# Performance work log

Hardware: AMD Instinct MI355X
Metric: run time of the kernel (lower is better)

## Reference

```python
import jax, jax.numpy as jnp
import numpy as np

B, S = 2, 2048
DIM_IN, DIM_OUT, NUM_HEADS, DIM_QK = 1024, 128, 16, 128


def setup_inputs() -> dict:
    key = jax.random.key(0)
    k0, k1, k2, k3 = jax.random.split(key, 4)
    x = jax.random.normal(k0, (B, S, DIM_IN), jnp.float32)
    mask = jax.random.bernoulli(k1, 0.1, (B, S))  # True = masked-out token
    # xavier-normal-ish scales (exact init values are irrelevant for correctness)
    std_in = float(np.sqrt(2.0 / (NUM_HEADS * DIM_QK + DIM_IN * DIM_QK)))
    proj_in = jax.random.normal(k2, (DIM_IN, NUM_HEADS, 2 * DIM_QK + DIM_OUT), jnp.float32) * std_in
    v_bias = jnp.zeros((NUM_HEADS, DIM_OUT), jnp.float32)
    std_out = float(np.sqrt(2.0 / (DIM_OUT * DIM_OUT + NUM_HEADS * DIM_OUT)))
    proj_out = jax.random.normal(k3, (NUM_HEADS, DIM_OUT, DIM_OUT), jnp.float32) * std_out
    proj_out_bias = jnp.zeros((DIM_OUT,), jnp.float32)
    return {"x": x, "mask": mask, "proj_in": proj_in, "v_bias": v_bias,
            "proj_out": proj_out, "proj_out_bias": proj_out_bias}


def _rotary(t):
    # t: [z, s, h, d]; GPT-NeoX style rotary as in the torch Rotary module
    d = t.shape[-1]
    half = -(-d // 2)  # ceil(d/2), matches torch.arange(0,-1,-2/d)
    freq_half = 10000.0 ** (jnp.arange(half, dtype=jnp.float32) * (-2.0 / d))
    freq = jnp.concatenate([freq_half, freq_half[: half - d % 2]])  # length d
    pos = jnp.arange(t.shape[1], dtype=jnp.float32)
    ang = pos[:, None] * freq[None, :]             # [s, d]
    cos = jnp.cos(ang)[None, :, None, :]
    sin = jnp.sin(ang)[None, :, None, :]
    x1, x2 = jnp.split(t, 2, axis=-1)
    rot = jnp.concatenate([-x2, x1], axis=-1)
    return t * cos + rot * sin


def _inf_cube(t):
    return t ** 3


def reference(x, mask, proj_in, v_bias, proj_out, proj_out_bias):
    qkv = jnp.einsum('zki,iho->zkho', x, proj_in)
    q, k, v = jnp.split(qkv, [DIM_QK, 2 * DIM_QK], axis=-1)
    q = _rotary(q)
    k = _rotary(k)
    scores = jnp.einsum('zqha,zkha->zqkh', q, k) / jnp.sqrt(jnp.float32(DIM_QK))
    # dual mask: row (query) OR column (key) masked -> -inf
    m = jnp.logical_or(mask[:, :, None, None], mask[:, None, :, None])  # [z,q,k,1]
    scores = jnp.where(m, -jnp.inf, scores)
    attn = jnp.nan_to_num(jax.nn.softmax(scores, axis=2))  # softmax over k; nan rows -> 0
    o = jnp.einsum('zqkh,zkhx->zqhx', attn, v + v_bias[None, None])
    out = jnp.einsum('zqhx,hxy->zqy', _inf_cube(o), proj_out) + proj_out_bias[None, None]
    return _inf_cube(out)
```

## Files before the change

kernel.cpp:

```cpp
#include <hip/hip_runtime.h>
#include <math.h>

#define BZ 2
#define SQ 2048
#define DIN 1024
#define HH 16
#define NT 6144
#define MROWS 4096
#define KOUT 2048
#define KSPLIT 8

typedef unsigned short u16t;
typedef unsigned int u32t;
typedef __attribute__((ext_vector_type(8))) short bf16x8;
typedef __attribute__((ext_vector_type(4))) float f32x4;

__device__ __forceinline__ float cubef(float x) { return x * x * x; }

__device__ __forceinline__ u16t f2bf(float f) {
    u32t b = __float_as_uint(f);
    b += 0x7FFFu + ((b >> 16) & 1u);
    return (u16t)(b >> 16);
}
__device__ __forceinline__ float bf2f(u16t u) { return __uint_as_float(((u32t)u) << 16); }
__device__ __forceinline__ u32t pk2(float a, float b) {
    return (u32t)f2bf(a) | ((u32t)f2bf(b) << 16);
}

__global__ __launch_bounds__(256) void bf16_x(const float* __restrict__ x,
                                              u16t* __restrict__ xb) {
    const size_t idx = ((size_t)blockIdx.x * 256 + threadIdx.x) * 8;
    float4 f0 = *(const float4*)&x[idx];
    float4 f1 = *(const float4*)&x[idx + 4];
    u32t h[4];
    h[0] = pk2(f0.x, f0.y); h[1] = pk2(f0.z, f0.w);
    h[2] = pk2(f1.x, f1.y); h[3] = pk2(f1.z, f1.w);
    *(uint4*)&xb[idx] = *(uint4*)&h[0];
}

__global__ __launch_bounds__(256) void transpose_w(const float* __restrict__ W,
                                                   u16t* __restrict__ Th) {
    __shared__ float tile[64][68];
    const int n0 = blockIdx.x * 64;
    const int k0 = blockIdx.y * 64;
    const int t = threadIdx.x;
    {
        const int r = t >> 4, c = (t & 15) * 4;
        #pragma unroll
        for (int p = 0; p < 4; p++) {
            float4 v = *(const float4*)&W[(size_t)(k0 + r + p * 16) * NT + n0 + c];
            *(float4*)&tile[r + p * 16][c] = v;
        }
    }
    __syncthreads();
    const int nr = t >> 2;
    const int kc = (t & 3) * 16;
    u32t hi[8];
    #pragma unroll
    for (int j = 0; j < 8; j++)
        hi[j] = pk2(tile[kc + 2 * j][nr], tile[kc + 2 * j + 1][nr]);
    size_t ob = (size_t)(n0 + nr) * DIN + k0 + kc;
    *(uint4*)&Th[ob]     = *(uint4*)&hi[0];
    *(uint4*)&Th[ob + 8] = *(uint4*)&hi[4];
}

__global__ __launch_bounds__(256) void transpose_w2(const float* __restrict__ W,
                                                    u16t* __restrict__ Th) {
    __shared__ float tile[64][68];
    const int n0 = blockIdx.x * 64;
    const int k0 = blockIdx.y * 64;
    const int t = threadIdx.x;
    {
        const int r = t >> 4, c = (t & 15) * 4;
        #pragma unroll
        for (int p = 0; p < 4; p++) {
            float4 v = *(const float4*)&W[(size_t)(k0 + r + p * 16) * 128 + n0 + c];
            *(float4*)&tile[r + p * 16][c] = v;
        }
    }
    __syncthreads();
    const int nr = t >> 2;
    const int kc = (t & 3) * 16;
    u32t hi[8];
    #pragma unroll
    for (int j = 0; j < 8; j++)
        hi[j] = pk2(tile[kc + 2 * j][nr], tile[kc + 2 * j + 1][nr]);
    size_t ob = (size_t)(n0 + nr) * KOUT + k0 + kc;
    *(uint4*)&Th[ob]     = *(uint4*)&hi[0];
    *(uint4*)&Th[ob + 8] = *(uint4*)&hi[4];
}

__global__ __launch_bounds__(256) void gemm_qkv3(const u16t* __restrict__ Ah,
                                                 const u16t* __restrict__ Bh,
                                                 const float* __restrict__ vb,
                                                 u16t* __restrict__ QB,
                                                 u16t* __restrict__ KB,
                                                 u16t* __restrict__ VF) {
    __shared__ __align__(16) u16t as_h[4 * 128 * 8];
    __shared__ __align__(16) u16t bs_h[4 * 128 * 8];

    const int t = threadIdx.x;
    const int lane = t & 63, wid = t >> 6;
    const int quad = lane >> 4, l15 = lane & 15;
    const int wm = (wid & 1) * 64;
    const int wn = (wid >> 1) * 64;
    const int tile = blockIdx.x;
    const int h = tile / 3, t3 = tile - h * 3;
    const int colBase = tile * 128;
    const int rowBase = blockIdx.y * 128;
    const int sm = t & 127;
    const int skh = t >> 7;

    f32x4 acc[4][4];
    #pragma unroll
    for (int i = 0; i < 4; i++)
        #pragma unroll
        for (int j = 0; j < 4; j++) acc[i][j] = (f32x4){0.f, 0.f, 0.f, 0.f};

    const u16t* aPtr = Ah + (size_t)(rowBase + sm) * DIN + skh * 16;
    const u16t* bPtr = Bh + (size_t)(colBase + sm) * DIN + skh * 16;
    u16t* aw = &as_h[(skh * 2) * 1024 + sm * 8];
    u16t* bw = &bs_h[(skh * 2) * 1024 + sm * 8];

    for (int k0 = 0; k0 < DIN; k0 += 32) {
        uint4 a0 = *(const uint4*)(aPtr + k0);
        uint4 a1 = *(const uint4*)(aPtr + k0 + 8);
        uint4 b0 = *(const uint4*)(bPtr + k0);
        uint4 b1 = *(const uint4*)(bPtr + k0 + 8);
        __syncthreads();
        *(uint4*)(aw)        = a0;
        *(uint4*)(aw + 1024) = a1;
        *(uint4*)(bw)        = b0;
        *(uint4*)(bw + 1024) = b1;
        __syncthreads();

        bf16x8 ah[4], bh[4];
        #pragma unroll
        for (int mt = 0; mt < 4; mt++)
            ah[mt] = *(const bf16x8*)&as_h[quad * 1024 + (wm + mt * 16 + l15) * 8];
        #pragma unroll
        for (int nt = 0; nt < 4; nt++)
            bh[nt] = *(const bf16x8*)&bs_h[quad * 1024 + (wn + nt * 16 + l15) * 8];
        #pragma unroll
        for (int mt = 0; mt < 4; mt++)
            #pragma unroll
            for (int nt = 0; nt < 4; nt++)
                acc[mt][nt] = __builtin_amdgcn_mfma_f32_16x16x32_bf16(ah[mt], bh[nt], acc[mt][nt], 0, 0, 0);
    }

    const int z = rowBase >> 11;
    const int s0 = (rowBase & 2047) + wm + quad * 4;
    const size_t obase = (size_t)(z * 16 + h) * 2048;
    if (t3 == 2) {
        #pragma unroll
        for (int nt = 0; nt < 4; nt++) {
            int c = wn + nt * 16 + l15;
            float bb = vb[h * 128 + c];
            #pragma unroll
            for (int mt = 0; mt < 4; mt++)
                #pragma unroll
                for (int r = 0; r < 4; r++)
                    VF[(obase + s0 + mt * 16 + r) * 128 + c] = f2bf(acc[mt][nt][r] + bb);
        }
    } else {
        u16t* dst = t3 ? KB : QB;
        #pragma unroll
        for (int nt = 0; nt < 4; nt++) {
            int c = wn + nt * 16 + l15;
            #pragma unroll
            for (int mt = 0; mt < 4; mt++)
                #pragma unroll
                for (int r = 0; r < 4; r++)
                    dst[(obase + s0 + mt * 16 + r) * 128 + c] = f2bf(acc[mt][nt][r]);
        }
    }
}

__global__ __launch_bounds__(256) void prep_rot_trans(u16t* __restrict__ QB,
                                                      u16t* __restrict__ KB,
                                                      u16t* __restrict__ VTh) {
    const int bx = blockIdx.x;
    const int st = bx & 63, h = (bx >> 6) & 15, z = bx >> 10;
    const int t = threadIdx.x;
    const size_t base = ((size_t)(z * 16 + h) * 2048 + st * 32) * 128;

    {
        const int r = t >> 3, w = t & 7;
        const int c = w & 3;
        const int s = st * 32 + r;
        u16t* buf = (w < 4) ? QB : KB;
        u16t* p1 = buf + base + (size_t)r * 128 + c * 16;
        u16t* p2 = p1 + 64;
        uint4 a0 = *(uint4*)p1, a1 = *(uint4*)(p1 + 8);
        uint4 b0 = *(uint4*)p2, b1 = *(uint4*)(p2 + 8);
        u32t A[8] = {a0.x, a0.y, a0.z, a0.w, a1.x, a1.y, a1.z, a1.w};
        u32t B[8] = {b0.x, b0.y, b0.z, b0.w, b1.x, b1.y, b1.z, b1.w};
        u32t OA[8], OB[8];
        #pragma unroll
        for (int p = 0; p < 8; p++) {
            float x1a = bf2f((u16t)(A[p] & 0xFFFFu)), x1b = bf2f((u16t)(A[p] >> 16));
            float x2a = bf2f((u16t)(B[p] & 0xFFFFu)), x2b = bf2f((u16t)(B[p] >> 16));
            int j0 = c * 16 + 2 * p;
            float f0 = expf(-0.14391156831212788f * (float)j0);
            float f1 = expf(-0.14391156831212788f * (float)(j0 + 1));
            float sn0, cs0, sn1, cs1;
            sincosf((float)s * f0, &sn0, &cs0);
            sincosf((float)s * f1, &sn1, &cs1);
            OA[p] = pk2(x1a * cs0 - x2a * sn0, x1b * cs1 - x2b * sn1);
            OB[p] = pk2(x2a * cs0 + x1a * sn0, x2b * cs1 + x1b * sn1);
        }
        *(uint4*)p1       = make_uint4(OA[0], OA[1], OA[2], OA[3]);
        *(uint4*)(p1 + 8) = make_uint4(OA[4], OA[5], OA[6], OA[7]);
        *(uint4*)p2       = make_uint4(OB[0], OB[1], OB[2], OB[3]);
        *(uint4*)(p2 + 8) = make_uint4(OB[4], OB[5], OB[6], OB[7]);
    }

    __shared__ u16t vt[128 * 40];
    {
        uint4 a = *(uint4*)(VTh + base + t * 16);
        uint4 b = *(uint4*)(VTh + base + t * 16 + 8);
        int row = t >> 3, d0 = (t & 7) * 16;
        u32t W[8] = {a.x, a.y, a.z, a.w, b.x, b.y, b.z, b.w};
        #pragma unroll
        for (int p = 0; p < 8; p++) {
            vt[(d0 + 2 * p) * 40 + row]     = (u16t)(W[p] & 0xFFFFu);
            vt[(d0 + 2 * p + 1) * 40 + row] = (u16t)(W[p] >> 16);
        }
    }
    __syncthreads();
    {
        int d = t >> 1, k0 = (t & 1) * 16;
        uint4 a = *(uint4*)&vt[d * 40 + k0];
        uint4 b = *(uint4*)&vt[d * 40 + k0 + 8];
        *(uint4*)(VTh + base + t * 16)     = a;
        *(uint4*)(VTh + base + t * 16 + 8) = b;
    }
}

#define ATTSCALE 0.08838834764831845f

__global__ __launch_bounds__(256, 4) void attn_kernel3(const u16t* __restrict__ QB,
                                                       const u16t* __restrict__ KB,
                                                       const u16t* __restrict__ VTh,
                                                       const int* __restrict__ mask,
                                                       u16t* __restrict__ O3b) {
    const int blk = blockIdx.x;
    const int qt = blk & 31;
    const int h  = (blk >> 5) & 15;
    const int z  = blk >> 9;
    const int t  = threadIdx.x;
    const int lane = t & 63, wid = t >> 6;
    const int quad = lane >> 4, l15 = lane & 15;
    const int w1 = wid & 1;
    const int kh = wid >> 1;

    __shared__ __align__(16) u16t ks[32 * 136];
    __shared__ __align__(16) u16t vth[128 * 40];
    __shared__ __align__(16) u16t wlb[64 * 40];
    __shared__ float dpart[2][64];
    __shared__ int qm[64], km[32];

    const int q0 = qt * 64;
    const size_t zh = (size_t)(z * 16 + h);
    const u16t* qb  = QB  + zh * 262144;
    const u16t* kb  = KB  + zh * 262144;
    const u16t* vhg = VTh + zh * 262144;

    bf16x8 qf[2][4];
    #pragma unroll
    for (int i = 0; i < 2; i++)
        #pragma unroll
        for (int kk = 0; kk < 4; kk++)
            qf[i][kk] = *(const bf16x8*)(qb + (size_t)(q0 + 16 * (w1 + 2 * i) + l15) * 128 + kk * 32 + quad * 8);
    if (t < 64) qm[t] = mask[z * SQ + q0 + t];

    f32x4 acc[2][4];
    #pragma unroll
    for (int i = 0; i < 2; i++)
        #pragma unroll
        for (int d = 0; d < 4; d++) acc[i][d] = (f32x4){0.f, 0.f, 0.f, 0.f};
    float dsum[2][4] = {{0.f, 0.f, 0.f, 0.f}, {0.f, 0.f, 0.f, 0.f}};

    for (int kt = 0; kt < SQ; kt += 32) {
        __syncthreads();
        {
            const u16t* src = kb + (size_t)kt * 128 + t * 16;
            uint4 a = *(const uint4*)(src);
            uint4 b = *(const uint4*)(src + 8);
            int row = t >> 3, co = (t & 7) * 16;
            *(uint4*)&ks[row * 136 + co]     = a;
            *(uint4*)&ks[row * 136 + co + 8] = b;
        }
        {
            const u16t* srch = vhg + (size_t)(kt >> 5) * 4096 + t * 16;
            uint4 a = *(const uint4*)(srch);
            uint4 b = *(const uint4*)(srch + 8);
            int dd = t >> 1, k0 = (t & 1) * 16;
            *(uint4*)&vth[dd * 40 + k0]     = a;
            *(uint4*)&vth[dd * 40 + k0 + 8] = b;
        }
        if (t < 32) km[t] = mask[z * SQ + kt + t];
        __syncthreads();

        f32x4 s4[2] = {(f32x4){0.f, 0.f, 0.f, 0.f}, (f32x4){0.f, 0.f, 0.f, 0.f}};
        #pragma unroll
        for (int kk = 0; kk < 4; kk++) {
            bf16x8 kf = *(const bf16x8*)&ks[(16 * kh + l15) * 136 + kk * 32 + quad * 8];
            s4[0] = __builtin_amdgcn_mfma_f32_16x16x32_bf16(qf[0][kk], kf, s4[0], 0, 0, 0);
            s4[1] = __builtin_amdgcn_mfma_f32_16x16x32_bf16(qf[1][kk], kf, s4[1], 0, 0, 0);
        }
        {
            int colm = km[16 * kh + l15];
            #pragma unroll
            for (int i = 0; i < 2; i++)
                #pragma unroll
                for (int r = 0; r < 4; r++) {
                    int row = 16 * (w1 + 2 * i) + 4 * quad + r;
                    float wv = (qm[row] | colm) ? 0.f : __expf(s4[i][r] * ATTSCALE);
                    dsum[i][r] += wv;
                    wlb[row * 40 + 16 * kh + l15] = f2bf(wv);
                }
        }
        __syncthreads();

        bf16x8 pa[2];
        #pragma unroll
        for (int i = 0; i < 2; i++)
            pa[i] = *(const bf16x8*)&wlb[(16 * (w1 + 2 * i) + l15) * 40 + quad * 8];
        #pragma unroll
        for (int dt = 0; dt < 4; dt++) {
            int d = 64 * kh + 16 * dt + l15;
            bf16x8 vh = *(const bf16x8*)&vth[d * 40 + quad * 8];
            acc[0][dt] = __builtin_amdgcn_mfma_f32_16x16x32_bf16(pa[0], vh, acc[0][dt], 0, 0, 0);
            acc[1][dt] = __builtin_amdgcn_mfma_f32_16x16x32_bf16(pa[1], vh, acc[1][dt], 0, 0, 0);
        }
    }

    #pragma unroll
    for (int i = 0; i < 2; i++)
        #pragma unroll
        for (int r = 0; r < 4; r++) {
            float v = dsum[i][r];
            v += __shfl_xor(v, 1);
            v += __shfl_xor(v, 2);
            v += __shfl_xor(v, 4);
            v += __shfl_xor(v, 8);
            dsum[i][r] = v;
        }
    if (l15 == 0) {
        #pragma unroll
        for (int i = 0; i < 2; i++)
            #pragma unroll
            for (int r = 0; r < 4; r++)
                dpart[kh][16 * (w1 + 2 * i) + 4 * quad + r] = dsum[i][r];
    }
    __syncthreads();

    #pragma unroll
    for (int i = 0; i < 2; i++)
        #pragma unroll
        for (int r = 0; r < 4; r++) {
            int row = 16 * (w1 + 2 * i) + 4 * quad + r;
            float den = dpart[0][row] + dpart[1][row];
            float inv = den > 0.f ? 1.f / den : 0.f;
            u16t* dst = O3b + (size_t)(z * SQ + q0 + row) * KOUT + h * 128 + 64 * kh;
            #pragma unroll
            for (int dt = 0; dt < 4; dt++)
                dst[16 * dt + l15] = f2bf(cubef(acc[i][dt][r] * inv));
        }
}

__global__ __launch_bounds__(256) void final_gemm2(const u16t* __restrict__ Ab,
                                                   const u16t* __restrict__ Bh,
                                                   float* __restrict__ part) {
    __shared__ __align__(16) u16t as_h[4 * 128 * 8];
    __shared__ __align__(16) u16t bs_h[4 * 128 * 8];

    const int t = threadIdx.x;
    const int lane = t & 63, wid = t >> 6;
    const int quad = lane >> 4, l15 = lane & 15;
    const int wm = (wid & 1) * 64;
    const int wn = (wid >> 1) * 64;
    const int rowBase = blockIdx.x * 128;
    const int kBase   = blockIdx.y * (KOUT / KSPLIT);
    const int sm = t & 127;
    const int skh = t >> 7;

    f32x4 acc[4][4];
    #pragma unroll
    for (int i = 0; i < 4; i++)
        #pragma unroll
        for (int j = 0; j < 4; j++) acc[i][j] = (f32x4){0.f, 0.f, 0.f, 0.f};

    const u16t* aPtr = Ab + (size_t)(rowBase + sm) * KOUT + kBase + skh * 16;
    const u16t* bPtr = Bh + (size_t)sm * KOUT + kBase + skh * 16;
    u16t* aw = &as_h[(skh * 2) * 1024 + sm * 8];
    u16t* bw = &bs_h[(skh * 2) * 1024 + sm * 8];

    for (int k0 = 0; k0 < KOUT / KSPLIT; k0 += 32) {
        uint4 a0 = *(const uint4*)(aPtr + k0);
        uint4 a1 = *(const uint4*)(aPtr + k0 + 8);
        uint4 b0 = *(const uint4*)(bPtr + k0);
        uint4 b1 = *(const uint4*)(bPtr + k0 + 8);
        __syncthreads();
        *(uint4*)(aw)        = a0;
        *(uint4*)(aw + 1024) = a1;
        *(uint4*)(bw)        = b0;
        *(uint4*)(bw + 1024) = b1;
        __syncthreads();

        bf16x8 ah[4], bh[4];
        #pragma unroll
        for (int mt = 0; mt < 4; mt++)
            ah[mt] = *(const bf16x8*)&as_h[quad * 1024 + (wm + mt * 16 + l15) * 8];
        #pragma unroll
        for (int nt = 0; nt < 4; nt++)
            bh[nt] = *(const bf16x8*)&bs_h[quad * 1024 + (wn + nt * 16 + l15) * 8];
        #pragma unroll
        for (int mt = 0; mt < 4; mt++)
            #pragma unroll
            for (int nt = 0; nt < 4; nt++)
                acc[mt][nt] = __builtin_amdgcn_mfma_f32_16x16x32_bf16(ah[mt], bh[nt], acc[mt][nt], 0, 0, 0);
    }

    float* pbase = part + (size_t)blockIdx.y * ((size_t)MROWS * 128);
    #pragma unroll
    for (int mt = 0; mt < 4; mt++)
        #pragma unroll
        for (int nt = 0; nt < 4; nt++) {
            int col = wn + nt * 16 + l15;
            #pragma unroll
            for (int r = 0; r < 4; r++) {
                int row = rowBase + wm + mt * 16 + quad * 4 + r;
                pbase[(size_t)row * 128 + col] = acc[mt][nt][r];
            }
        }
}

__global__ __launch_bounds__(256) void reduce_bias_cube(const float* __restrict__ part,
                                                        const float* __restrict__ bias,
                                                        float* __restrict__ out) {
    const int idx = (blockIdx.x * 256 + threadIdx.x) * 4;
    float4 s = {0.f, 0.f, 0.f, 0.f};
    #pragma unroll
    for (int p = 0; p < KSPLIT; p++) {
        float4 v = *(const float4*)&part[(size_t)p * ((size_t)MROWS * 128) + idx];
        s.x += v.x; s.y += v.y; s.z += v.z; s.w += v.w;
    }
    float4 b = *(const float4*)&bias[idx & 127];
    float4 r;
    r.x = cubef(s.x + b.x);
    r.y = cubef(s.y + b.y);
    r.z = cubef(s.z + b.z);
    r.w = cubef(s.w + b.w);
    *(float4*)&out[idx] = r;
}

extern "C" void kernel_launch(void* const* d_in, const int* in_sizes, int n_in,
                              void* d_out, int out_size, void* d_ws, size_t ws_size,
                              hipStream_t stream) {
    const float* x        = (const float*)d_in[0];
    const int*   mask     = (const int*)d_in[1];
    const float* proj_in  = (const float*)d_in[2];
    const float* v_bias   = (const float*)d_in[3];
    const float* proj_out = (const float*)d_in[4];
    const float* po_bias  = (const float*)d_in[5];
    float* out = (float*)d_out;

    u16t* QB  = (u16t*)d_ws;
    u16t* KB  = QB + (size_t)8388608;
    u16t* VTh = KB + (size_t)8388608;
    u16t* xb  = VTh + (size_t)8388608;
    u16t* O3b = xb + (size_t)4194304;
    u16t* pTh = O3b;
    u16t* WTh = QB;
    float* partials = (float*)(WTh + (size_t)128 * KOUT);

    bf16_x<<<(MROWS * DIN) / (256 * 8), 256, 0, stream>>>(x, xb);
    transpose_w<<<dim3(NT / 64, DIN / 64), 256, 0, stream>>>(proj_in, pTh);
    gemm_qkv3<<<dim3(48, MROWS / 128), 256, 0, stream>>>(xb, pTh, v_bias, QB, KB, VTh);
    prep_rot_trans<<<BZ * HH * (SQ / 32), 256, 0, stream>>>(QB, KB, VTh);
    attn_kernel3<<<BZ * HH * (SQ / 64), 256, 0, stream>>>(QB, KB, VTh, mask, O3b);
    transpose_w2<<<dim3(2, KOUT / 64), 256, 0, stream>>>(proj_out, WTh);
    final_gemm2<<<dim3(MROWS / 128, KSPLIT), 256, 0, stream>>>(O3b, WTh, partials);
    reduce_bias_cube<<<(MROWS * 128) / (256 * 4), 256, 0, stream>>>(partials, po_bias, out);
}
```

Baseline: 347.4 us.

## Retile attention to 128-query blocks with per-wave full key and head-dim ownership

The attention kernel now processes 128 query rows per block instead of 64. Each wave owns 32 query rows across all 32 keys of a tile and the full 128-wide head dimension, so every K/V tile staged in LDS serves twice as many queries. Because each wave writes and reads only its own rows of the probability buffer, the mid-iteration barrier and the cross-wave denominator reduction through shared memory are gone. In exchange the grid is halved to 512 blocks, the accumulator doubles to 64 floats per lane, and the occupancy hint drops to 3, which could hurt latency hiding and load balance.

```diff
diff --git a/kernel.cpp b/kernel.cpp
--- a/kernel.cpp
+++ b/kernel.cpp
@@ -239,28 +239,25 @@
 
 #define ATTSCALE 0.08838834764831845f
 
-__global__ __launch_bounds__(256, 4) void attn_kernel3(const u16t* __restrict__ QB,
+__global__ __launch_bounds__(256, 3) void attn_kernel4(const u16t* __restrict__ QB,
                                                        const u16t* __restrict__ KB,
                                                        const u16t* __restrict__ VTh,
                                                        const int* __restrict__ mask,
                                                        u16t* __restrict__ O3b) {
     const int blk = blockIdx.x;
-    const int qt = blk & 31;
-    const int h  = (blk >> 5) & 15;
-    const int z  = blk >> 9;
+    const int qt = blk & 15;
+    const int h  = (blk >> 4) & 15;
+    const int z  = blk >> 8;
     const int t  = threadIdx.x;
     const int lane = t & 63, wid = t >> 6;
     const int quad = lane >> 4, l15 = lane & 15;
-    const int w1 = wid & 1;
-    const int kh = wid >> 1;
 
     __shared__ __align__(16) u16t ks[32 * 136];
     __shared__ __align__(16) u16t vth[128 * 40];
-    __shared__ __align__(16) u16t wlb[64 * 40];
-    __shared__ float dpart[2][64];
-    __shared__ int qm[64], km[32];
-
-    const int q0 = qt * 64;
+    __shared__ __align__(16) u16t wlb[128 * 40];
+    __shared__ int qm[128], km[32];
+
+    const int q0 = qt * 128;
     const size_t zh = (size_t)(z * 16 + h);
     const u16t* qb  = QB  + zh * 262144;
     const u16t* kb  = KB  + zh * 262144;
@@ -271,14 +268,14 @@
     for (int i = 0; i < 2; i++)
         #pragma unroll
         for (int kk = 0; kk < 4; kk++)
-            qf[i][kk] = *(const bf16x8*)(qb + (size_t)(q0 + 16 * (w1 + 2 * i) + l15) * 128 + kk * 32 + quad * 8);
-    if (t < 64) qm[t] = mask[z * SQ + q0 + t];
-
-    f32x4 acc[2][4];
+            qf[i][kk] = *(const bf16x8*)(qb + (size_t)(q0 + 16 * (2 * wid + i) + l15) * 128 + kk * 32 + quad * 8);
+    if (t < 128) qm[t] = mask[z * SQ + q0 + t];
+
+    f32x4 acc[2][8];
     #pragma unroll
     for (int i = 0; i < 2; i++)
         #pragma unroll
-        for (int d = 0; d < 4; d++) acc[i][d] = (f32x4){0.f, 0.f, 0.f, 0.f};
+        for (int d = 0; d < 8; d++) acc[i][d] = (f32x4){0.f, 0.f, 0.f, 0.f};
     float dsum[2][4] = {{0.f, 0.f, 0.f, 0.f}, {0.f, 0.f, 0.f, 0.f}};
 
     for (int kt = 0; kt < SQ; kt += 32) {
@@ -302,35 +299,42 @@
         if (t < 32) km[t] = mask[z * SQ + kt + t];
         __syncthreads();
 
-        f32x4 s4[2] = {(f32x4){0.f, 0.f, 0.f, 0.f}, (f32x4){0.f, 0.f, 0.f, 0.f}};
+        f32x4 s4[2][2];
+        #pragma unroll
+        for (int i = 0; i < 2; i++)
+            #pragma unroll
+            for (int n = 0; n < 2; n++) s4[i][n] = (f32x4){0.f, 0.f, 0.f, 0.f};
         #pragma unroll
         for (int kk = 0; kk < 4; kk++) {
-            bf16x8 kf = *(const bf16x8*)&ks[(16 * kh + l15) * 136 + kk * 32 + quad * 8];
-            s4[0] = __builtin_amdgcn_mfma_f32_16x16x32_bf16(qf[0][kk], kf, s4[0], 0, 0, 0);
-            s4[1] = __builtin_amdgcn_mfma_f32_16x16x32_bf16(qf[1][kk], kf, s4[1], 0, 0, 0);
+            bf16x8 kf0 = *(const bf16x8*)&ks[l15 * 136 + kk * 32 + quad * 8];
+            bf16x8 kf1 = *(const bf16x8*)&ks[(16 + l15) * 136 + kk * 32 + quad * 8];
+            s4[0][0] = __builtin_amdgcn_mfma_f32_16x16x32_bf16(qf[0][kk], kf0, s4[0][0], 0, 0, 0);
+            s4[0][1] = __builtin_amdgcn_mfma_f32_16x16x32_bf16(qf[0][kk], kf1, s4[0][1], 0, 0, 0);
+            s4[1][0] = __builtin_amdgcn_mfma_f32_16x16x32_bf16(qf[1][kk], kf0, s4[1][0], 0, 0, 0);
+            s4[1][1] = __builtin_amdgcn_mfma_f32_16x16x32_bf16(qf[1][kk], kf1, s4[1][1], 0, 0, 0);
         }
         {
-            int colm = km[16 * kh + l15];
+            int colm0 = km[l15], colm1 = km[16 + l15];
             #pragma unroll
             for (int i = 0; i < 2; i++)
                 #pragma unroll
                 for (int r = 0; r < 4; r++) {
-                    int row = 16 * (w1 + 2 * i) + 4 * quad + r;
-                    float wv = (qm[row] | colm) ? 0.f : __expf(s4[i][r] * ATTSCALE);
-                    dsum[i][r] += wv;
-                    wlb[row * 40 + 16 * kh + l15] = f2bf(wv);
+                    int row = 16 * (2 * wid + i) + 4 * quad + r;
+                    int qmr = qm[row];
+                    float w0 = (qmr | colm0) ? 0.f : __expf(s4[i][0][r] * ATTSCALE);
+                    float w1 = (qmr | colm1) ? 0.f : __expf(s4[i][1][r] * ATTSCALE);
+                    dsum[i][r] += w0 + w1;
+                    wlb[row * 40 + l15]      = f2bf(w0);
+                    wlb[row * 40 + 16 + l15] = f2bf(w1);
                 }
         }
-        __syncthreads();
-
         bf16x8 pa[2];
         #pragma unroll
         for (int i = 0; i < 2; i++)
-            pa[i] = *(const bf16x8*)&wlb[(16 * (w1 + 2 * i) + l15) * 40 + quad * 8];
-        #pragma unroll
-        for (int dt = 0; dt < 4; dt++) {
-            int d = 64 * kh + 16 * dt + l15;
-            bf16x8 vh = *(const bf16x8*)&vth[d * 40 + quad * 8];
+            pa[i] = *(const bf16x8*)&wlb[(16 * (2 * wid + i) + l15) * 40 + quad * 8];
+        #pragma unroll
+        for (int dt = 0; dt < 8; dt++) {
+            bf16x8 vh = *(const bf16x8*)&vth[(16 * dt + l15) * 40 + quad * 8];
             acc[0][dt] = __builtin_amdgcn_mfma_f32_16x16x32_bf16(pa[0], vh, acc[0][dt], 0, 0, 0);
             acc[1][dt] = __builtin_amdgcn_mfma_f32_16x16x32_bf16(pa[1], vh, acc[1][dt], 0, 0, 0);
         }
@@ -347,25 +351,17 @@
             v += __shfl_xor(v, 8);
             dsum[i][r] = v;
         }
-    if (l15 == 0) {
-        #pragma unroll
-        for (int i = 0; i < 2; i++)
-            #pragma unroll
-            for (int r = 0; r < 4; r++)
-                dpart[kh][16 * (w1 + 2 * i) + 4 * quad + r] = dsum[i][r];
-    }
-    __syncthreads();
 
     #pragma unroll
     for (int i = 0; i < 2; i++)
         #pragma unroll
         for (int r = 0; r < 4; r++) {
-            int row = 16 * (w1 + 2 * i) + 4 * quad + r;
-            float den = dpart[0][row] + dpart[1][row];
+            int row = 16 * (2 * wid + i) + 4 * quad + r;
+            float den = dsum[i][r];
             float inv = den > 0.f ? 1.f / den : 0.f;
-            u16t* dst = O3b + (size_t)(z * SQ + q0 + row) * KOUT + h * 128 + 64 * kh;
-            #pragma unroll
-            for (int dt = 0; dt < 4; dt++)
+            u16t* dst = O3b + (size_t)(z * SQ + q0 + row) * KOUT + h * 128;
+            #pragma unroll
+            for (int dt = 0; dt < 8; dt++)
                 dst[16 * dt + l15] = f2bf(cubef(acc[i][dt][r] * inv));
         }
 }
@@ -480,7 +476,7 @@
     transpose_w<<<dim3(NT / 64, DIN / 64), 256, 0, stream>>>(proj_in, pTh);
     gemm_qkv3<<<dim3(48, MROWS / 128), 256, 0, stream>>>(xb, pTh, v_bias, QB, KB, VTh);
     prep_rot_trans<<<BZ * HH * (SQ / 32), 256, 0, stream>>>(QB, KB, VTh);
-    attn_kernel3<<<BZ * HH * (SQ / 64), 256, 0, stream>>>(QB, KB, VTh, mask, O3b);
+    attn_kernel4<<<BZ * HH * (SQ / 128), 256, 0, stream>>>(QB, KB, VTh, mask, O3b);
     transpose_w2<<<dim3(2, KOUT / 64), 256, 0, stream>>>(proj_out, WTh);
     final_gemm2<<<dim3(MROWS / 128, KSPLIT), 256, 0, stream>>>(O3b, WTh, partials);
     reduce_bias_cube<<<(MROWS * 128) / (256 * 4), 256, 0, stream>>>(partials, po_bias, out);
```

Result: no change. 344.6 us (-0.8%).
